# Performance work log

Measured on AMD Instinct MI355X. Metric: run time of the kernel, lower is better.

The kernel has to match this reference:

```python
import jax, jax.numpy as jnp
import numpy as np

HEADS = 20  # head_dim = 1280 // 20 = 64
LORA_SCALE = 1.0


def setup_inputs() -> dict:
    key = jax.random.key(0)
    ks = jax.random.split(key, 16)
    B, S, C, R = 2, 2048, 1280, 4
    w = 0.02  # keep activations numerically tame
    inp = {
        "x": jax.random.normal(ks[0], (B, S, C), jnp.float32),
        "Wq": jax.random.normal(ks[1], (C, C), jnp.float32) * w,
        "Wk": jax.random.normal(ks[2], (C, C), jnp.float32) * w,
        "Wv": jax.random.normal(ks[3], (C, C), jnp.float32) * w,
        "Wo": jax.random.normal(ks[4], (C, C), jnp.float32) * w,
        "bo": jnp.zeros((C,), jnp.float32),
        "Aq": jax.random.normal(ks[5], (R, C), jnp.float32) * w,
        "Bq": jax.random.normal(ks[6], (C, R), jnp.float32) * w,
        "Ak": jax.random.normal(ks[7], (R, C), jnp.float32) * w,
        "Bk": jax.random.normal(ks[8], (C, R), jnp.float32) * w,
        "Av": jax.random.normal(ks[9], (R, C), jnp.float32) * w,
        "Bv": jax.random.normal(ks[10], (C, R), jnp.float32) * w,
        "Ao": jax.random.normal(ks[11], (R, C), jnp.float32) * w,
        "Bo": jax.random.normal(ks[12], (C, R), jnp.float32) * w,
    }
    return inp


def _lora(x, A, B):
    # LoRALinearLayer: up(down(x)); network_alpha=None -> no extra scaling
    return (x @ A.T) @ B.T


def reference(x, Wq, Wk, Wv, Wo, bo, Aq, Bq, Ak, Bk, Av, Bv, Ao, Bo):
    B, S, C = x.shape
    H = HEADS
    D = C // H
    # base projections + LoRA updates (self-attention: encoder_hidden_states = x)
    q = x @ Wq.T + LORA_SCALE * _lora(x, Aq, Bq)
    k = x @ Wk.T + LORA_SCALE * _lora(x, Ak, Bk)
    v = x @ Wv.T + LORA_SCALE * _lora(x, Av, Bv)
    # head split: [B, S, H, D]
    q = q.reshape(B, S, H, D)
    k = k.reshape(B, S, H, D)
    v = v.reshape(B, S, H, D)
    # explicit scores + softmax (attn.get_attention_scores), scale = 1/sqrt(D)
    scale = 1.0 / jnp.sqrt(jnp.asarray(D, x.dtype))
    scores = jnp.einsum("bshd,bthd->bhst", q, k) * scale  # [B, H, S, S]
    probs = jax.nn.softmax(scores, axis=-1)
    ctx = jnp.einsum("bhst,bthd->bshd", probs, v).reshape(B, S, C)
    # output projection (+bias) + LoRA; dropout is identity at eval
    out = ctx @ Wo.T + bo + LORA_SCALE * _lora(ctx, Ao, Bo)
    return out
```

## Files before the change

### kernel.cpp

```cpp
#include <hip/hip_runtime.h>

#define BATCH 2
#define SEQ   2048
#define CH    1280
#define NH    20
#define HD    64
#define BS    (BATCH*SEQ)
#define RK    4

typedef __attribute__((ext_vector_type(2)))  float floatx2;
typedef __attribute__((ext_vector_type(4)))  short bf16x4;
typedef __attribute__((ext_vector_type(8)))  short bf16x8;
typedef __attribute__((ext_vector_type(16))) float floatx16;

__device__ __forceinline__ floatx16 mfma32(bf16x8 a, bf16x8 b, floatx16 c) {
    return __builtin_amdgcn_mfma_f32_32x32x16_bf16(a, b, c, 0, 0, 0);
}

__device__ __forceinline__ unsigned short f2bf(float f) {
    unsigned int u = __float_as_uint(f);
    u += 0x7fffu + ((u >> 16) & 1u);
    return (unsigned short)(u >> 16);
}
__device__ __forceinline__ unsigned int packbf(float hi, float lo) {
    unsigned int a = __float_as_uint(hi) + 0x8000u;
    unsigned int b = __float_as_uint(lo) + 0x8000u;
    return __builtin_amdgcn_perm(a, b, 0x07060302u);
}
__device__ __forceinline__ float fexp2(float x) {
#if __has_builtin(__builtin_amdgcn_exp2f)
    return __builtin_amdgcn_exp2f(x);
#else
    return exp2f(x);
#endif
}

__device__ __forceinline__ void cp16(const unsigned short* g, unsigned short* l) {
    __builtin_amdgcn_global_load_lds(
        (const __attribute__((address_space(1))) unsigned int*)g,
        (__attribute__((address_space(3))) unsigned int*)l, 16, 0, 0);
}

#define F4_BLOCKS   (CH * CH / 1024)
#define CAST_BLOCKS (BS * CH / 1024)

__global__ __launch_bounds__(256) void prep(
    const float* __restrict__ x,
    const float* __restrict__ Wq, const float* __restrict__ Wk,
    const float* __restrict__ Wv, const float* __restrict__ Wo,
    const float* __restrict__ Aq, const float* __restrict__ Bq,
    const float* __restrict__ Ak, const float* __restrict__ Bk,
    const float* __restrict__ Av, const float* __restrict__ Bv,
    const float* __restrict__ Ao, const float* __restrict__ Bo,
    unsigned short* __restrict__ wq_bf, unsigned short* __restrict__ wk_bf,
    unsigned short* __restrict__ wv_bf, unsigned short* __restrict__ wo_bf,
    unsigned short* __restrict__ xb)
{
    const int bx = blockIdx.x;
    if (bx < 4 * F4_BLOCKS) {
        int which = bx / F4_BLOCKS;
        int e = ((bx % F4_BLOCKS) * 256 + threadIdx.x) * 4;
        int i = e / CH, j = e % CH;
        const float *W, *A, *Bm;
        unsigned short* o;
        if (which == 0)      { W = Wq; A = Aq; Bm = Bq; o = wq_bf; }
        else if (which == 1) { W = Wk; A = Ak; Bm = Bk; o = wk_bf; }
        else if (which == 2) { W = Wv; A = Av; Bm = Bv; o = wv_bf; }
        else                 { W = Wo; A = Ao; Bm = Bo; o = wo_bf; }
        float4 acc = *(const float4*)(W + e);
#pragma unroll
        for (int r = 0; r < RK; r++) {
            float bm = Bm[i * RK + r];
            float4 a4 = *(const float4*)(A + r * CH + j);
            acc.x += bm * a4.x; acc.y += bm * a4.y;
            acc.z += bm * a4.z; acc.w += bm * a4.w;
        }
        ushort4 ov;
        ov.x = f2bf(acc.x); ov.y = f2bf(acc.y);
        ov.z = f2bf(acc.z); ov.w = f2bf(acc.w);
        *(ushort4*)(o + e) = ov;
    } else {
        int idx = ((bx - 4 * F4_BLOCKS) * 256 + threadIdx.x) * 4;
        float4 v = *(const float4*)(x + idx);
        ushort4 o;
        o.x = f2bf(v.x); o.y = f2bf(v.y); o.z = f2bf(v.z); o.w = f2bf(v.w);
        *(ushort4*)(xb + idx) = o;
    }
}

__device__ __forceinline__ void gemm128(
    const unsigned short* __restrict__ A, const unsigned short* __restrict__ B,
    unsigned short* __restrict__ obf, float* __restrict__ of,
    const float* __restrict__ bias, float oscale, int mode,
    unsigned short* __restrict__ vt)
{
    __shared__ __align__(16) unsigned short smem[2 * 128 * 64];
    unsigned short* sa = smem;
    unsigned short* sb = smem + 128 * 64;
    const int tid = threadIdx.x;
    const int wav = tid >> 6, lane = tid & 63;
    const int n32 = lane & 31, half = lane >> 5;
    const int wr = wav >> 1, wc = wav & 1;
    const int M0 = blockIdx.y * 128, N0 = blockIdx.x * 128;

    const unsigned short* ga[4]; const unsigned short* gb[4];
    unsigned short* la[4]; unsigned short* lb[4];
#pragma unroll
    for (int g = 0; g < 4; g++) {
        int s = g * 256 + tid;
        int row = s >> 3, cc = (s & 7) ^ (row & 7);
        ga[g] = A + (size_t)(M0 + row) * CH + cc * 8;
        gb[g] = B + (size_t)(N0 + row) * CH + cc * 8;
        la[g] = sa + (size_t)(g * 256 + wav * 64) * 8;
        lb[g] = sb + (size_t)(g * 256 + wav * 64) * 8;
    }

    const int arow0 = wr * 64 + n32, brow0 = wc * 64 + n32;

    floatx16 acc[2][2];
#pragma unroll
    for (int mt = 0; mt < 2; mt++)
#pragma unroll
        for (int nt = 0; nt < 2; nt++)
#pragma unroll
            for (int r = 0; r < 16; r++) acc[mt][nt][r] = 0.f;

    for (int k0 = 0; k0 < CH; k0 += 64) {
#pragma unroll
        for (int g = 0; g < 4; g++) { cp16(ga[g], la[g]); cp16(gb[g], lb[g]); }
#pragma unroll
        for (int g = 0; g < 4; g++) { ga[g] += 64; gb[g] += 64; }
        __syncthreads();

        bf16x8 av[2][4], bv[2][4];
#pragma unroll
        for (int mt = 0; mt < 2; mt++) {
            const int ar = arow0 + mt * 32, br = brow0 + mt * 32;
#pragma unroll
            for (int ks = 0; ks < 4; ks++) {
                const int cc = ks * 2 + half;
                av[mt][ks] = *(const bf16x8*)(sa + ar * 64 + ((cc ^ (ar & 7)) << 3));
                bv[mt][ks] = *(const bf16x8*)(sb + br * 64 + ((cc ^ (br & 7)) << 3));
            }
        }
#pragma unroll
        for (int ks = 0; ks < 4; ks++)
#pragma unroll
            for (int mt = 0; mt < 2; mt++)
#pragma unroll
                for (int nt = 0; nt < 2; nt++)
                    acc[mt][nt] = mfma32(av[mt][ks], bv[nt][ks], acc[mt][nt]);
        __syncthreads();
    }

    if (mode == 2) {
#pragma unroll
        for (int mt = 0; mt < 2; mt++) {
#pragma unroll
            for (int nt = 0; nt < 2; nt++) {
                const int dl = wc * 64 + nt * 32 + n32;
#pragma unroll
                for (int j = 0; j < 4; j++) {
                    const int u = wr * 16 + mt * 8 + 2 * j + half;
                    uint2 w;
                    w.x = packbf(acc[mt][nt][4 * j + 1], acc[mt][nt][4 * j + 0]);
                    w.y = packbf(acc[mt][nt][4 * j + 3], acc[mt][nt][4 * j + 2]);
                    *(uint2*)(smem + dl * 128 + ((u ^ n32) << 2)) = w;
                }
            }
        }
        __syncthreads();
        const int b = M0 >> 11;
        const int s_in = M0 & (SEQ - 1);
#pragma unroll
        for (int g = 0; g < 8; g++) {
            int cid = g * 256 + tid;
            int dl = cid >> 4, pc = cid & 15;
            int g32 = pc >> 2, p = (pc & 3) >> 1, hb = pc & 1;
            int u1 = 8 * g32 + 4 * p + 2 * hb;
            int sw = dl & 31;
            uint2 r1 = *(const uint2*)(smem + dl * 128 + ((u1 ^ sw) << 2));
            uint2 r2 = *(const uint2*)(smem + dl * 128 + (((u1 + 1) ^ sw) << 2));
            int ch = N0 + dl, h = ch >> 6, d = ch & 63;
            uint4 val; val.x = r1.x; val.y = r1.y; val.z = r2.x; val.w = r2.y;
            *(uint4*)(vt + (size_t)((b * NH + h) * HD + d) * SEQ + s_in + pc * 8) = val;
        }
        return;
    }

#pragma unroll
    for (int mt = 0; mt < 2; mt++) {
#pragma unroll
        for (int nt = 0; nt < 2; nt++) {
            const int col = N0 + wc * 64 + nt * 32 + n32;
            const float bv2 = (mode == 1) ? bias[col] : 0.f;
#pragma unroll
            for (int r = 0; r < 16; r++) {
                size_t row = (size_t)(M0 + wr * 64 + mt * 32 +
                                      (r & 3) + 8 * (r >> 2) + 4 * half);
                if (mode == 1) of[row * CH + col] = acc[mt][nt][r] + bv2;
                else           obf[row * CH + col] = f2bf(acc[mt][nt][r] * oscale);
            }
        }
    }
}

__global__ __launch_bounds__(256) void gemm_qkv(
    const unsigned short* __restrict__ xb,
    const unsigned short* __restrict__ wq, const unsigned short* __restrict__ wk,
    const unsigned short* __restrict__ wv,
    unsigned short* __restrict__ q, unsigned short* __restrict__ k,
    unsigned short* __restrict__ vt)
{
    const unsigned short* w = blockIdx.z == 0 ? wq : blockIdx.z == 1 ? wk : wv;
    unsigned short* o = blockIdx.z == 0 ? q : k;
    float scale = blockIdx.z == 0 ? 0.18033688011112042f : 1.0f;
    int mode = blockIdx.z == 2 ? 2 : 0;
    gemm128(xb, w, o, nullptr, nullptr, scale, mode, vt);
}

__global__ __launch_bounds__(256) void gemm_o(
    const unsigned short* __restrict__ c_bf, const unsigned short* __restrict__ wo,
    const float* __restrict__ bias, float* __restrict__ out)
{
    gemm128(c_bf, wo, nullptr, out, bias, 1.0f, 1, nullptr);
}

__global__ __launch_bounds__(512, 4) void attention(
    const unsigned short* __restrict__ q, const unsigned short* __restrict__ k,
    const unsigned short* __restrict__ vt, unsigned short* __restrict__ c_bf)
{
    __shared__ __align__(16) unsigned short smem[2 * (128 * 64 + 64 * 128)];

    const int tid = threadIdx.x, wav = tid >> 6, lane = tid & 63;
    const int n32 = lane & 31, half = lane >> 5;
    const int qg = wav >> 1, kh = wav & 1;
    const int q0 = blockIdx.x * 128;
    const int bh = blockIdx.y, b = bh / NH, h = bh % NH;

    const size_t qrow = (size_t)(b * SEQ + q0 + qg * 32 + n32);
    bf16x8 qf[4];
#pragma unroll
    for (int f = 0; f < 4; f++)
        qf[f] = *(const bf16x8*)(q + qrow * CH + h * HD + f * 16 + half * 8);

    const int rowk = tid >> 3, cck = (tid & 7) ^ (rowk & 7);
    const int rowv = tid >> 4, ccv = (tid & 15) ^ (rowv & 15);
    const unsigned short* gk0 = k + (size_t)(b * SEQ + rowk) * CH + h * HD + cck * 8;
    const unsigned short* gv0 = vt + (size_t)(bh * HD + rowv) * SEQ + ccv * 8;

    auto STAGE = [&](int t, int bufb) {
        const unsigned short* gk = gk0 + (size_t)t * 128 * CH;
        const unsigned short* gv = gv0 + t * 128;
        unsigned short* lk = smem + bufb * 16384 + wav * 512;
        unsigned short* lv = smem + bufb * 16384 + 8192 + wav * 512;
#pragma unroll
        for (int g = 0; g < 2; g++) {
            cp16(gk + (size_t)g * 64 * CH, lk + g * 4096);
            cp16(gv + (size_t)g * 32 * SEQ, lv + g * 4096);
        }
    };

    floatx2 ps = {0.f, 0.f};
    floatx16 acc[2];
#pragma unroll
    for (int dt = 0; dt < 2; dt++)
#pragma unroll
        for (int r = 0; r < 16; r++) acc[dt][r] = 0.f;

    auto COMPUTE = [&](int bufb) {
        const unsigned short* k_lds = smem + bufb * 16384;
        const unsigned short* v_lds = k_lds + 8192;
#pragma unroll
        for (int ktl = 0; ktl < 2; ktl++) {
            const int kt = kh * 2 + ktl;
            const int keyrow = kt * 32 + n32;
            const unsigned short* kr = k_lds + keyrow * 64;
            floatx16 st;
#pragma unroll
            for (int r = 0; r < 16; r++) st[r] = 0.f;
#pragma unroll
            for (int f = 0; f < 4; f++) {
                int phys = (2 * f + half) ^ (keyrow & 7);
                bf16x8 kf = *(const bf16x8*)(kr + phys * 8);
                st = mfma32(kf, qf[f], st);
            }

#pragma unroll
            for (int pp = 0; pp < 2; pp++) {
                float p[8];
#pragma unroll
                for (int r = 0; r < 8; r++) p[r] = fexp2(st[8 * pp + r]);
#pragma unroll
                for (int j = 0; j < 4; j++)
                    ps += (floatx2){p[2 * j], p[2 * j + 1]};
                unsigned int lo0 = packbf(p[1], p[0]);
                unsigned int lo1 = packbf(p[3], p[2]);
                unsigned int hi0 = packbf(p[5], p[4]);
                unsigned int hi1 = packbf(p[7], p[6]);
                asm volatile("v_permlane32_swap_b32 %0, %1"
                             : "+v"(lo0), "+v"(hi0));
                asm volatile("v_permlane32_swap_b32 %0, %1"
                             : "+v"(lo1), "+v"(hi1));
                union { unsigned int u[4]; bf16x8 v; } pb;
                pb.u[0] = lo0; pb.u[1] = lo1; pb.u[2] = hi0; pb.u[3] = hi1;
                const int ct = kt * 4 + pp * 2 + half;
#pragma unroll
                for (int dt = 0; dt < 2; dt++) {
                    const int drow = dt * 32 + n32;
                    int phys = ct ^ (drow & 15);
                    bf16x8 vv = *(const bf16x8*)(v_lds + drow * 128 + phys * 8);
                    acc[dt] = mfma32(vv, pb.v, acc[dt]);
                }
            }
        }
    };

    STAGE(0, 0);
    for (int it = 0; it < 15; it++) {
        STAGE(it + 1, (it + 1) & 1);
        asm volatile("s_waitcnt vmcnt(4)" ::: "memory");
        __builtin_amdgcn_s_barrier();
        __builtin_amdgcn_sched_barrier(0);
        COMPUTE(it & 1);
        __builtin_amdgcn_s_barrier();
    }
    asm volatile("s_waitcnt vmcnt(0)" ::: "memory");
    __builtin_amdgcn_s_barrier();
    __builtin_amdgcn_sched_barrier(0);
    COMPUTE(1);

    float psum = ps.x + ps.y;
    float* ex = (float*)smem;
#pragma unroll
    for (int p2 = 0; p2 < 2; p2++) {
        __syncthreads();
        if (kh == 1 && (qg >> 1) == p2) {
            float* dst = ex + (size_t)((qg & 1) * 64 + lane) * 33;
#pragma unroll
            for (int dt = 0; dt < 2; dt++)
#pragma unroll
                for (int r = 0; r < 16; r++) dst[dt * 16 + r] = acc[dt][r];
            dst[32] = psum;
        }
        __syncthreads();
        if (kh == 0 && (qg >> 1) == p2) {
            const float* src = ex + (size_t)((qg & 1) * 64 + lane) * 33;
#pragma unroll
            for (int dt = 0; dt < 2; dt++)
#pragma unroll
                for (int r = 0; r < 16; r++) acc[dt][r] += src[dt * 16 + r];
            psum += src[32];
        }
    }
    if (kh) return;

    float tot = psum + __shfl_xor(psum, 32, 64);
    float rinv = __frcp_rn(tot);
    const size_t obase = qrow * CH + h * HD;
#pragma unroll
    for (int dt = 0; dt < 2; dt++) {
#pragma unroll
        for (int jj = 0; jj < 4; jj++) {
            int d = dt * 32 + 8 * jj + 4 * half;
            uint2 o2;
            o2.x = packbf(acc[dt][4 * jj + 1] * rinv, acc[dt][4 * jj + 0] * rinv);
            o2.y = packbf(acc[dt][4 * jj + 3] * rinv, acc[dt][4 * jj + 2] * rinv);
            *(uint2*)(c_bf + obase + d) = o2;
        }
    }
}

extern "C" void kernel_launch(void* const* d_in, const int* in_sizes, int n_in,
                              void* d_out, int out_size, void* d_ws, size_t ws_size,
                              hipStream_t stream)
{
    const float* x  = (const float*)d_in[0];
    const float* Wq = (const float*)d_in[1];
    const float* Wk = (const float*)d_in[2];
    const float* Wv = (const float*)d_in[3];
    const float* Wo = (const float*)d_in[4];
    const float* bo = (const float*)d_in[5];
    const float* Aq = (const float*)d_in[6];
    const float* Bq = (const float*)d_in[7];
    const float* Ak = (const float*)d_in[8];
    const float* Bk = (const float*)d_in[9];
    const float* Av = (const float*)d_in[10];
    const float* Bv = (const float*)d_in[11];
    const float* Ao = (const float*)d_in[12];
    const float* Bo = (const float*)d_in[13];
    float* out = (float*)d_out;

    char* ws = (char*)d_ws;
    size_t off = 0;
    auto alloc = [&](size_t bytes) -> void* {
        void* p = ws + off; off += (bytes + 255) & ~(size_t)255; return p;
    };
    const size_t WB = (size_t)CH * CH, XB = (size_t)BS * CH;
    unsigned short* wq_bf = (unsigned short*)alloc(WB * 2);
    unsigned short* wk_bf = (unsigned short*)alloc(WB * 2);
    unsigned short* wv_bf = (unsigned short*)alloc(WB * 2);
    unsigned short* wo_bf = (unsigned short*)alloc(WB * 2);
    unsigned short* x_bf  = (unsigned short*)alloc(XB * 2);
    unsigned short* q_bf  = (unsigned short*)alloc(XB * 2);
    unsigned short* k_bf  = (unsigned short*)alloc(XB * 2);
    unsigned short* vt_bf = (unsigned short*)alloc(XB * 2);
    unsigned short* c_bf  = (unsigned short*)alloc(XB * 2);
    (void)ws_size; (void)n_in; (void)in_sizes; (void)out_size;

    prep<<<dim3(4 * F4_BLOCKS + CAST_BLOCKS), 256, 0, stream>>>(
        x, Wq, Wk, Wv, Wo, Aq, Bq, Ak, Bk, Av, Bv, Ao, Bo,
        wq_bf, wk_bf, wv_bf, wo_bf, x_bf);

    gemm_qkv<<<dim3(CH / 128, BS / 128, 3), 256, 0, stream>>>(
        x_bf, wq_bf, wk_bf, wv_bf, q_bf, k_bf, vt_bf);

    attention<<<dim3(SEQ / 128, BATCH * NH), 512, 0, stream>>>(
        q_bf, k_bf, vt_bf, c_bf);

    gemm_o<<<dim3(CH / 128, BS / 128), 256, 0, stream>>>(c_bf, wo_bf, bo, out);
}
```

Measured before the change: 256.8 us.

## Software-pipeline QK and softmax-PV across tiles with triple-buffered V

Splits the attention inner loop into separate QK and softmax+PV stages and staggers them, so the QK MFMAs for the next key subtile are issued while the exp/pack work of the previous one runs. V is now triple-buffered in LDS (K stays double-buffered) so V from the previous tile stays valid while the next is staged. It also raises wave priority around the MFMA bursts with s_setprio. The change costs more LDS (40 KB versus 32 KB) and holds an extra score accumulator in registers, which could reduce occupancy.

```diff
diff --git a/kernel.cpp b/kernel.cpp
--- a/kernel.cpp
+++ b/kernel.cpp
@@ -230,7 +230,7 @@
     const unsigned short* __restrict__ q, const unsigned short* __restrict__ k,
     const unsigned short* __restrict__ vt, unsigned short* __restrict__ c_bf)
 {
-    __shared__ __align__(16) unsigned short smem[2 * (128 * 64 + 64 * 128)];
+    __shared__ __align__(16) unsigned short smem[5 * 8192];
 
     const int tid = threadIdx.x, wav = tid >> 6, lane = tid & 63;
     const int n32 = lane & 31, half = lane >> 5;
@@ -249,11 +249,11 @@
     const unsigned short* gk0 = k + (size_t)(b * SEQ + rowk) * CH + h * HD + cck * 8;
     const unsigned short* gv0 = vt + (size_t)(bh * HD + rowv) * SEQ + ccv * 8;
 
-    auto STAGE = [&](int t, int bufb) {
+    auto STAGE = [&](int t) {
         const unsigned short* gk = gk0 + (size_t)t * 128 * CH;
         const unsigned short* gv = gv0 + t * 128;
-        unsigned short* lk = smem + bufb * 16384 + wav * 512;
-        unsigned short* lv = smem + bufb * 16384 + 8192 + wav * 512;
+        unsigned short* lk = smem + (t & 1) * 8192 + wav * 512;
+        unsigned short* lv = smem + 16384 + (t % 3) * 8192 + wav * 512;
 #pragma unroll
         for (int g = 0; g < 2; g++) {
             cp16(gk + (size_t)g * 64 * CH, lk + g * 4096);
@@ -268,67 +268,83 @@
 #pragma unroll
         for (int r = 0; r < 16; r++) acc[dt][r] = 0.f;
 
-    auto COMPUTE = [&](int bufb) {
-        const unsigned short* k_lds = smem + bufb * 16384;
-        const unsigned short* v_lds = k_lds + 8192;
-#pragma unroll
-        for (int ktl = 0; ktl < 2; ktl++) {
-            const int kt = kh * 2 + ktl;
-            const int keyrow = kt * 32 + n32;
-            const unsigned short* kr = k_lds + keyrow * 64;
-            floatx16 st;
-#pragma unroll
-            for (int r = 0; r < 16; r++) st[r] = 0.f;
-#pragma unroll
-            for (int f = 0; f < 4; f++) {
-                int phys = (2 * f + half) ^ (keyrow & 7);
-                bf16x8 kf = *(const bf16x8*)(kr + phys * 8);
-                st = mfma32(kf, qf[f], st);
+    auto QK = [&](int t, int ktl, floatx16& st) {
+        const unsigned short* k_lds = smem + (t & 1) * 8192;
+        const int keyrow = (kh * 2 + ktl) * 32 + n32;
+        const unsigned short* kr = k_lds + keyrow * 64;
+#pragma unroll
+        for (int r = 0; r < 16; r++) st[r] = 0.f;
+        __builtin_amdgcn_s_setprio(1);
+#pragma unroll
+        for (int f = 0; f < 4; f++) {
+            int phys = (2 * f + half) ^ (keyrow & 7);
+            bf16x8 kf = *(const bf16x8*)(kr + phys * 8);
+            st = mfma32(kf, qf[f], st);
+        }
+        __builtin_amdgcn_s_setprio(0);
+    };
+
+    auto SMPV = [&](int t, int ktl, const floatx16& st) {
+        const unsigned short* v_lds = smem + 16384 + (t % 3) * 8192;
+        const int kt = kh * 2 + ktl;
+#pragma unroll
+        for (int pp = 0; pp < 2; pp++) {
+            float p[8];
+#pragma unroll
+            for (int r = 0; r < 8; r++) p[r] = fexp2(st[8 * pp + r]);
+#pragma unroll
+            for (int j = 0; j < 4; j++)
+                ps += (floatx2){p[2 * j], p[2 * j + 1]};
+            unsigned int lo0 = packbf(p[1], p[0]);
+            unsigned int lo1 = packbf(p[3], p[2]);
+            unsigned int hi0 = packbf(p[5], p[4]);
+            unsigned int hi1 = packbf(p[7], p[6]);
+            asm volatile("v_permlane32_swap_b32 %0, %1" : "+v"(lo0), "+v"(hi0));
+            asm volatile("v_permlane32_swap_b32 %0, %1" : "+v"(lo1), "+v"(hi1));
+            union { unsigned int u[4]; bf16x8 v; } pb;
+            pb.u[0] = lo0; pb.u[1] = lo1; pb.u[2] = hi0; pb.u[3] = hi1;
+            const int ct = kt * 4 + pp * 2 + half;
+            __builtin_amdgcn_s_setprio(1);
+#pragma unroll
+            for (int dt = 0; dt < 2; dt++) {
+                const int drow = dt * 32 + n32;
+                int phys = ct ^ (drow & 15);
+                bf16x8 vv = *(const bf16x8*)(v_lds + drow * 128 + phys * 8);
+                acc[dt] = mfma32(vv, pb.v, acc[dt]);
             }
-
-#pragma unroll
-            for (int pp = 0; pp < 2; pp++) {
-                float p[8];
-#pragma unroll
-                for (int r = 0; r < 8; r++) p[r] = fexp2(st[8 * pp + r]);
-#pragma unroll
-                for (int j = 0; j < 4; j++)
-                    ps += (floatx2){p[2 * j], p[2 * j + 1]};
-                unsigned int lo0 = packbf(p[1], p[0]);
-                unsigned int lo1 = packbf(p[3], p[2]);
-                unsigned int hi0 = packbf(p[5], p[4]);
-                unsigned int hi1 = packbf(p[7], p[6]);
-                asm volatile("v_permlane32_swap_b32 %0, %1"
-                             : "+v"(lo0), "+v"(hi0));
-                asm volatile("v_permlane32_swap_b32 %0, %1"
-                             : "+v"(lo1), "+v"(hi1));
-                union { unsigned int u[4]; bf16x8 v; } pb;
-                pb.u[0] = lo0; pb.u[1] = lo1; pb.u[2] = hi0; pb.u[3] = hi1;
-                const int ct = kt * 4 + pp * 2 + half;
-#pragma unroll
-                for (int dt = 0; dt < 2; dt++) {
-                    const int drow = dt * 32 + n32;
-                    int phys = ct ^ (drow & 15);
-                    bf16x8 vv = *(const bf16x8*)(v_lds + drow * 128 + phys * 8);
-                    acc[dt] = mfma32(vv, pb.v, acc[dt]);
-                }
-            }
+            __builtin_amdgcn_s_setprio(0);
         }
     };
 
-    STAGE(0, 0);
-    for (int it = 0; it < 15; it++) {
-        STAGE(it + 1, (it + 1) & 1);
+    floatx16 stX, stY;
+    STAGE(0); STAGE(1);
+    asm volatile("s_waitcnt vmcnt(4)" ::: "memory");
+    __builtin_amdgcn_s_barrier();
+    __builtin_amdgcn_sched_barrier(0);
+    QK(0, 0, stY);
+    QK(0, 1, stX);
+    SMPV(0, 0, stY);
+    __builtin_amdgcn_s_barrier();
+#pragma unroll
+    for (int t = 1; t < 15; t++) {
+        STAGE(t + 1);
         asm volatile("s_waitcnt vmcnt(4)" ::: "memory");
         __builtin_amdgcn_s_barrier();
         __builtin_amdgcn_sched_barrier(0);
-        COMPUTE(it & 1);
+        QK(t, 0, stY);
+        SMPV(t - 1, 1, stX);
+        QK(t, 1, stX);
+        SMPV(t, 0, stY);
         __builtin_amdgcn_s_barrier();
     }
     asm volatile("s_waitcnt vmcnt(0)" ::: "memory");
     __builtin_amdgcn_s_barrier();
     __builtin_amdgcn_sched_barrier(0);
-    COMPUTE(1);
+    QK(15, 0, stY);
+    SMPV(14, 1, stX);
+    QK(15, 1, stX);
+    SMPV(15, 0, stY);
+    SMPV(15, 1, stX);
 
     float psum = ps.x + ps.y;
     float* ex = (float*)smem;
```

Result: no change. 257.0 us (+0.1%).

## Halve attention key tile to 64 and raise occupancy to eight blocks

Applied to the files above, without the earlier changes.

Each attention iteration now stages and processes 64 keys instead of 128, so the double-buffered LDS shrinks to 32 KB. The launch-bounds minimum-blocks hint rises from 4 to 8, and the V swizzle is adjusted to the narrower 64-column tile. The aim is more resident waves per CU to hide memory and exp latency. In exchange the kernel runs twice as many pipeline iterations with their barriers and waitcnts, and tighter register limits could cause spills.

```diff
diff --git a/kernel.cpp b/kernel.cpp
--- a/kernel.cpp
+++ b/kernel.cpp
@@ -226,11 +226,11 @@
     gemm128(c_bf, wo, nullptr, out, bias, 1.0f, 1, nullptr);
 }
 
-__global__ __launch_bounds__(512, 4) void attention(
+__global__ __launch_bounds__(512, 8) void attention(
     const unsigned short* __restrict__ q, const unsigned short* __restrict__ k,
     const unsigned short* __restrict__ vt, unsigned short* __restrict__ c_bf)
 {
-    __shared__ __align__(16) unsigned short smem[2 * (128 * 64 + 64 * 128)];
+    __shared__ __align__(16) unsigned short smem[2 * 8192];
 
     const int tid = threadIdx.x, wav = tid >> 6, lane = tid & 63;
     const int n32 = lane & 31, half = lane >> 5;
@@ -245,20 +245,17 @@
         qf[f] = *(const bf16x8*)(q + qrow * CH + h * HD + f * 16 + half * 8);
 
     const int rowk = tid >> 3, cck = (tid & 7) ^ (rowk & 7);
-    const int rowv = tid >> 4, ccv = (tid & 15) ^ (rowv & 15);
+    const int ccv = (tid & 7) ^ (rowk & 7);
     const unsigned short* gk0 = k + (size_t)(b * SEQ + rowk) * CH + h * HD + cck * 8;
-    const unsigned short* gv0 = vt + (size_t)(bh * HD + rowv) * SEQ + ccv * 8;
-
-    auto STAGE = [&](int t, int bufb) {
-        const unsigned short* gk = gk0 + (size_t)t * 128 * CH;
-        const unsigned short* gv = gv0 + t * 128;
-        unsigned short* lk = smem + bufb * 16384 + wav * 512;
-        unsigned short* lv = smem + bufb * 16384 + 8192 + wav * 512;
-#pragma unroll
-        for (int g = 0; g < 2; g++) {
-            cp16(gk + (size_t)g * 64 * CH, lk + g * 4096);
-            cp16(gv + (size_t)g * 32 * SEQ, lv + g * 4096);
-        }
+    const unsigned short* gv0 = vt + (size_t)(bh * HD + rowk) * SEQ + ccv * 8;
+
+    auto STAGE = [&](int t) {
+        const unsigned short* gk = gk0 + (size_t)t * 64 * CH;
+        const unsigned short* gv = gv0 + (t >> 1) * 128 + (t & 1) * 64;
+        unsigned short* lk = smem + (t & 1) * 8192 + wav * 512;
+        unsigned short* lv = smem + (t & 1) * 8192 + 4096 + wav * 512;
+        cp16(gk, lk);
+        cp16(gv, lv);
     };
 
     floatx2 ps = {0.f, 0.f};
@@ -268,67 +265,60 @@
 #pragma unroll
         for (int r = 0; r < 16; r++) acc[dt][r] = 0.f;
 
-    auto COMPUTE = [&](int bufb) {
-        const unsigned short* k_lds = smem + bufb * 16384;
-        const unsigned short* v_lds = k_lds + 8192;
-#pragma unroll
-        for (int ktl = 0; ktl < 2; ktl++) {
-            const int kt = kh * 2 + ktl;
-            const int keyrow = kt * 32 + n32;
-            const unsigned short* kr = k_lds + keyrow * 64;
-            floatx16 st;
-#pragma unroll
-            for (int r = 0; r < 16; r++) st[r] = 0.f;
-#pragma unroll
-            for (int f = 0; f < 4; f++) {
-                int phys = (2 * f + half) ^ (keyrow & 7);
-                bf16x8 kf = *(const bf16x8*)(kr + phys * 8);
-                st = mfma32(kf, qf[f], st);
+    auto COMPUTE = [&](int t) {
+        const unsigned short* k_lds = smem + (t & 1) * 8192;
+        const unsigned short* v_lds = k_lds + 4096;
+        const int keyrow = kh * 32 + n32;
+        const unsigned short* kr = k_lds + keyrow * 64;
+        floatx16 st;
+#pragma unroll
+        for (int r = 0; r < 16; r++) st[r] = 0.f;
+#pragma unroll
+        for (int f = 0; f < 4; f++) {
+            int phys = (2 * f + half) ^ (keyrow & 7);
+            bf16x8 kf = *(const bf16x8*)(kr + phys * 8);
+            st = mfma32(kf, qf[f], st);
+        }
+#pragma unroll
+        for (int pp = 0; pp < 2; pp++) {
+            float p[8];
+#pragma unroll
+            for (int r = 0; r < 8; r++) p[r] = fexp2(st[8 * pp + r]);
+#pragma unroll
+            for (int j = 0; j < 4; j++)
+                ps += (floatx2){p[2 * j], p[2 * j + 1]};
+            unsigned int lo0 = packbf(p[1], p[0]);
+            unsigned int lo1 = packbf(p[3], p[2]);
+            unsigned int hi0 = packbf(p[5], p[4]);
+            unsigned int hi1 = packbf(p[7], p[6]);
+            asm volatile("v_permlane32_swap_b32 %0, %1" : "+v"(lo0), "+v"(hi0));
+            asm volatile("v_permlane32_swap_b32 %0, %1" : "+v"(lo1), "+v"(hi1));
+            union { unsigned int u[4]; bf16x8 v; } pb;
+            pb.u[0] = lo0; pb.u[1] = lo1; pb.u[2] = hi0; pb.u[3] = hi1;
+            const int ct = kh * 4 + pp * 2 + half;
+#pragma unroll
+            for (int dt = 0; dt < 2; dt++) {
+                const int drow = dt * 32 + n32;
+                int phys = ct ^ (drow & 7);
+                bf16x8 vv = *(const bf16x8*)(v_lds + drow * 64 + phys * 8);
+                acc[dt] = mfma32(vv, pb.v, acc[dt]);
             }
-
-#pragma unroll
-            for (int pp = 0; pp < 2; pp++) {
-                float p[8];
-#pragma unroll
-                for (int r = 0; r < 8; r++) p[r] = fexp2(st[8 * pp + r]);
-#pragma unroll
-                for (int j = 0; j < 4; j++)
-                    ps += (floatx2){p[2 * j], p[2 * j + 1]};
-                unsigned int lo0 = packbf(p[1], p[0]);
-                unsigned int lo1 = packbf(p[3], p[2]);
-                unsigned int hi0 = packbf(p[5], p[4]);
-                unsigned int hi1 = packbf(p[7], p[6]);
-                asm volatile("v_permlane32_swap_b32 %0, %1"
-                             : "+v"(lo0), "+v"(hi0));
-                asm volatile("v_permlane32_swap_b32 %0, %1"
-                             : "+v"(lo1), "+v"(hi1));
-                union { unsigned int u[4]; bf16x8 v; } pb;
-                pb.u[0] = lo0; pb.u[1] = lo1; pb.u[2] = hi0; pb.u[3] = hi1;
-                const int ct = kt * 4 + pp * 2 + half;
-#pragma unroll
-                for (int dt = 0; dt < 2; dt++) {
-                    const int drow = dt * 32 + n32;
-                    int phys = ct ^ (drow & 15);
-                    bf16x8 vv = *(const bf16x8*)(v_lds + drow * 128 + phys * 8);
-                    acc[dt] = mfma32(vv, pb.v, acc[dt]);
-                }
-            }
         }
     };
 
-    STAGE(0, 0);
-    for (int it = 0; it < 15; it++) {
-        STAGE(it + 1, (it + 1) & 1);
-        asm volatile("s_waitcnt vmcnt(4)" ::: "memory");
+    STAGE(0);
+    for (int t = 0; t < 31; t++) {
+        STAGE(t + 1);
+        asm volatile("s_waitcnt vmcnt(2)" ::: "memory");
         __builtin_amdgcn_s_barrier();
         __builtin_amdgcn_sched_barrier(0);
-        COMPUTE(it & 1);
+        COMPUTE(t);
         __builtin_amdgcn_s_barrier();
     }
     asm volatile("s_waitcnt vmcnt(0)" ::: "memory");
     __builtin_amdgcn_s_barrier();
     __builtin_amdgcn_sched_barrier(0);
-    COMPUTE(1);
+    COMPUTE(31);
 
     float psum = ps.x + ps.y;
     float* ex = (float*)smem;
```

New measurement: 557.2 us. 117% more time.
